# Kernel optimization log

Hardware: AMD Instinct MI355X
Metric: run time of the kernel (lower is better)

The kernel has to match this reference:

```python
import jax, jax.numpy as jnp
import numpy as np

N = 100000      # nodes (single ntype)
R = 4           # edge types (relations)
E = 160000      # edges per relation
D_IN = 128
D_OUT = 128


def setup_inputs() -> dict:
    key = jax.random.key(0)
    k1, k2, k3, k4, k5 = jax.random.split(key, 5)
    gain = np.sqrt(2.0)  # calculate_gain('relu')
    bound = gain * np.sqrt(6.0 / (D_IN + D_OUT))  # xavier_uniform
    return {
        "x": jax.random.normal(k1, (N, D_IN), dtype=jnp.float32),
        "weight": jax.random.uniform(k2, (R, D_IN, D_OUT), dtype=jnp.float32,
                                     minval=-bound, maxval=bound),
        "loop_weight": jax.random.uniform(k3, (D_IN, D_OUT), dtype=jnp.float32,
                                          minval=-bound, maxval=bound),
        "h_bias": jnp.zeros((D_OUT,), dtype=jnp.float32),
        "src_idx": jax.random.randint(k4, (R, E), 0, N),
        "dst_idx": jax.random.randint(k5, (R, E), 0, N),
    }


def reference(x, weight, loop_weight, h_bias, src_idx, dst_idx):
    # Per-relation GraphConv(norm='right', weight external):
    #   h_r = segment_sum((x @ W_r)[src], dst) / clamp(in_degree, 1)
    # HeteroGraphConv default aggregation sums relations per dst node.
    n = x.shape[0]
    xw = jnp.einsum('nd,rdo->rno', x, weight)  # [R, N, D_OUT]
    h = jnp.zeros((n, weight.shape[2]), dtype=x.dtype)
    ones = jnp.ones((src_idx.shape[1],), dtype=x.dtype)
    for r in range(weight.shape[0]):  # small fixed relation count
        msg = xw[r][src_idx[r]]                                   # [E, D_OUT]
        agg = jax.ops.segment_sum(msg, dst_idx[r], num_segments=n)
        deg = jax.ops.segment_sum(ones, dst_idx[r], num_segments=n)
        h = h + agg / jnp.clip(deg, 1.0)[:, None]                 # norm='right'
    # self-loop + bias + activation (dropout=0 -> identity)
    h = h + x @ loop_weight + h_bias
    return jax.nn.relu(h)
```

## Files before the change

### kernel.cpp

```cpp
#include <hip/hip_runtime.h>

#define DD 128
#define KY 512
#define KT 640
#define RR 4
#define BKT 16
#define CAPS 15
#define NKS (KT / 32)

typedef short short8 __attribute__((ext_vector_type(8)));
typedef float f32x4 __attribute__((ext_vector_type(4)));

union U4S8 { uint4 u; short8 s; };

__device__ __forceinline__ unsigned short f2bf(float f) {
  unsigned u = __float_as_uint(f);
  u += 0x7fffu + ((u >> 16) & 1u);
  return (unsigned short)(u >> 16);
}

__global__ __launch_bounds__(256) void prep(const float* __restrict__ x,
                                            const float* __restrict__ weight,
                                            const float* __restrict__ loopw,
                                            const int* __restrict__ src,
                                            const int* __restrict__ dst,
                                            unsigned short* __restrict__ xb,
                                            unsigned short* __restrict__ wt,
                                            int* __restrict__ slot,
                                            int N, int E, int FB, int XB) {
  int b = blockIdx.x;
  int t = threadIdx.x;
  if (b < FB) {
    int i = b * 256 + t;
    if (i >= RR * E) return;
    int r = i / E;
    size_t base = ((size_t)dst[i] * RR + r) * BKT;
    int pos = atomicAdd(slot + base, 1);
    if (pos < CAPS) slot[base + 1 + pos] = src[i];
  } else if (b < FB + XB) {
    int i = (b - FB) * 256 + t;
    if (i >= (N + 1) * 16) return;
    int n = i >> 4;
    uint4 o = make_uint4(0, 0, 0, 0);
    if (n < N) {
      const float4* xp = (const float4*)x + (size_t)i * 2;
      float4 v0 = xp[0], v1 = xp[1];
      o.x = (unsigned)f2bf(v0.x) | ((unsigned)f2bf(v0.y) << 16);
      o.y = (unsigned)f2bf(v0.z) | ((unsigned)f2bf(v0.w) << 16);
      o.z = (unsigned)f2bf(v1.x) | ((unsigned)f2bf(v1.y) << 16);
      o.w = (unsigned)f2bf(v1.z) | ((unsigned)f2bf(v1.w) << 16);
    }
    ((uint4*)xb)[i] = o;
  } else {
    int i = (b - FB - XB) * 256 + t;
    if (i >= DD * KT) return;
    int j = i & 7, l = (i >> 3) & 63, c = (i >> 9) & 7, ks = i >> 12;
    int k = ks * 32 + (l >> 4) * 8 + j;
    int col = c * 16 + (l & 15);
    float v = (k < KY) ? weight[(size_t)((k >> 7) * DD + (k & (DD - 1))) * DD + col]
                       : loopw[(size_t)(k - KY) * DD + col];
    wt[i] = f2bf(v);
  }
}

__global__ __launch_bounds__(256) void gather_agg(const unsigned* __restrict__ xbu,
                                                  const int* __restrict__ slot,
                                                  unsigned* __restrict__ yu,
                                                  int NN ) {
  int gid = blockIdx.x * 256 + threadIdx.x;
  int n = gid >> 6, lane = gid & 63;
  if (n >= NN) return;
  int N = NN - 1;

  int sv = slot[(size_t)n * 64 + lane];

  int cn[RR], ct[RR];
#pragma unroll
  for (int r = 0; r < RR; r++) {
    ct[r] = __builtin_amdgcn_readlane(sv, r << 4);
    cn[r] = ct[r] > CAPS ? CAPS : ct[r];
  }

  float ax[RR], ay[RR];
#pragma unroll
  for (int r = 0; r < RR; r++) { ax[r] = 0.f; ay[r] = 0.f; }

#pragma unroll
  for (int r = 0; r < RR; r++) {
    for (int u = 0; u < cn[r]; u += 2) {
      int s0 = __builtin_amdgcn_readlane(sv, (r << 4) + 1 + u);
      int s1 = __builtin_amdgcn_readlane(sv, (r << 4) + 2 + u);
      s1 = (u + 1 < cn[r]) ? s1 : N;
      unsigned v0 = xbu[(size_t)s0 * 64 + lane];
      unsigned v1 = xbu[(size_t)s1 * 64 + lane];
      ax[r] += __uint_as_float(v0 << 16);
      ay[r] += __uint_as_float(v0 & 0xffff0000u);
      ax[r] += __uint_as_float(v1 << 16);
      ay[r] += __uint_as_float(v1 & 0xffff0000u);
    }
  }

#pragma unroll
  for (int r = 0; r < RR; r++) {
    float inv = 1.0f / (float)max(ct[r], 1);
    yu[(size_t)n * (KY / 2) + r * 64 + lane] =
        (unsigned)f2bf(ax[r] * inv) | ((unsigned)f2bf(ay[r] * inv) << 16);
  }
}

__global__ __launch_bounds__(512) void gemm_mfma(const unsigned short* __restrict__ y,
                                                 const unsigned short* __restrict__ xb,
                                                 const uint4* __restrict__ wtv,
                                                 const float* __restrict__ bias,
                                                 float* __restrict__ out, int N) {
  __shared__ __align__(16) unsigned short Bs[2][4096];
  int t = threadIdx.x;
  int w = t >> 6, lane = t & 63;
  int m = lane & 15, q = lane >> 4;
  int rb = blockIdx.x * 256;

  int grow0 = rb + w * 32 + m, grow1 = grow0 + 16;
  int r0c = grow0 > N ? N : grow0;
  int r1c = grow1 > N ? N : grow1;
  const unsigned short* ay0 = y  + (size_t)r0c * KY + q * 8;
  const unsigned short* ay1 = y  + (size_t)r1c * KY + q * 8;
  const unsigned short* ax0 = xb + (size_t)r0c * DD + q * 8;
  const unsigned short* ax1 = xb + (size_t)r1c * DD + q * 8;

  *(uint4*)(&Bs[0][t * 8]) = wtv[t];
  __syncthreads();

  f32x4 acc[2][8];
#pragma unroll
  for (int i = 0; i < 2; i++)
#pragma unroll
    for (int c = 0; c < 8; c++) acc[i][c] = (f32x4){0.f, 0.f, 0.f, 0.f};

#pragma unroll
  for (int ks = 0; ks < NKS; ++ks) {
    const int buf = ks & 1;
    uint4 bs;
    if (ks + 1 < NKS) bs = wtv[(size_t)(ks + 1) * 512 + t];

    U4S8 a0, a1;
    if (ks < 16) {
      a0.u = *(const uint4*)(ay0 + ks * 32);
      a1.u = *(const uint4*)(ay1 + ks * 32);
    } else {
      a0.u = *(const uint4*)(ax0 + (ks - 16) * 32);
      a1.u = *(const uint4*)(ax1 + (ks - 16) * 32);
    }

    short8 bb[8];
#pragma unroll
    for (int c = 0; c < 8; ++c)
      bb[c] = *(const short8*)(&Bs[buf][(c * 64 + lane) * 8]);

#pragma unroll
    for (int c = 0; c < 8; ++c) {
      acc[0][c] = __builtin_amdgcn_mfma_f32_16x16x32_bf16(a0.s, bb[c], acc[0][c], 0, 0, 0);
      acc[1][c] = __builtin_amdgcn_mfma_f32_16x16x32_bf16(a1.s, bb[c], acc[1][c], 0, 0, 0);
    }

    if (ks + 1 < NKS) {
      *(uint4*)(&Bs[buf ^ 1][t * 8]) = bs;
      __syncthreads();
    }
  }

  float bv[8];
#pragma unroll
  for (int c = 0; c < 8; ++c) bv[c] = bias[c * 16 + m];
#pragma unroll
  for (int i = 0; i < 2; ++i) {
    int rbase = rb + w * 32 + i * 16 + q * 4;
#pragma unroll
    for (int v = 0; v < 4; ++v) {
      int gr = rbase + v;
      if (gr < N) {
#pragma unroll
        for (int c = 0; c < 8; ++c)
          out[(size_t)gr * DD + c * 16 + m] = fmaxf(acc[i][c][v] + bv[c], 0.f);
      }
    }
  }
}

extern "C" void kernel_launch(void* const* d_in, const int* in_sizes, int n_in,
                              void* d_out, int out_size, void* d_ws, size_t ws_size,
                              hipStream_t stream) {
  const float* x      = (const float*)d_in[0];
  const float* weight = (const float*)d_in[1];
  const float* loop_w = (const float*)d_in[2];
  const float* h_bias = (const float*)d_in[3];
  const int*   src    = (const int*)d_in[4];
  const int*   dst    = (const int*)d_in[5];
  float* out = (float*)d_out;

  const int N = in_sizes[0] / DD;
  const int R = in_sizes[1] / (DD * DD);
  const int E = in_sizes[4] / R;
  const int RE = R * E;

  char* p = (char*)d_ws;
  auto alloc = [&](size_t bytes) {
    char* q = p;
    p += (bytes + 63) & ~size_t(63);
    return q;
  };
  int* slot = (int*)alloc((size_t)(N + 1) * RR * BKT * 4);
  unsigned short* wt = (unsigned short*)alloc((size_t)DD * KT * 2);
  unsigned short* xb = (unsigned short*)alloc((size_t)(N + 1) * DD * 2);
  unsigned short* y  = (unsigned short*)alloc((size_t)(N + 1) * KY * 2);

  hipMemsetAsync(slot, 0, (size_t)(N + 1) * RR * BKT * 4, stream);

  int FB = (RE + 255) / 256;
  int XB = ((N + 1) * 16 + 255) / 256;
  int WB = (DD * KT + 255) / 256;
  prep<<<FB + XB + WB, 256, 0, stream>>>(x, weight, loop_w, src, dst,
                                         xb, wt, slot, N, E, FB, XB);
  gather_agg<<<((size_t)(N + 1) * 64 + 255) / 256, 256, 0, stream>>>(
      (const unsigned*)xb, slot, (unsigned*)y, N + 1);
  gemm_mfma<<<(N + 255) / 256, 512, 0, stream>>>(y, xb, (const uint4*)wt,
                                                 h_bias, out, N);
}
```

Measured before the change: 226.7 us.

## Fuse memset, prep, gather and GEMM into one cooperative persistent kernel

Replaces the memset and three separate kernel launches with a single cooperative kernel. Each stage becomes a grid-stride loop, and grid.sync() separates slot zeroing, bucketing/conversion, aggregation and the MFMA GEMM. The aim is to remove launch overhead and inter-kernel gaps. In exchange the grid is capped at 512 persistent blocks, adds three grid-wide barriers, and could lower parallelism in the gather stage compared with the earlier one-wave-per-node launch.

```diff
diff --git a/kernel.cpp b/kernel.cpp
--- a/kernel.cpp
+++ b/kernel.cpp
@@ -1,4 +1,7 @@
 #include <hip/hip_runtime.h>
+#include <hip/hip_cooperative_groups.h>
+
+namespace cg = cooperative_groups;
 
 #define DD 128
 #define KY 512
@@ -19,168 +22,171 @@
   return (unsigned short)(u >> 16);
 }
 
-__global__ __launch_bounds__(256) void prep(const float* __restrict__ x,
-                                            const float* __restrict__ weight,
-                                            const float* __restrict__ loopw,
-                                            const int* __restrict__ src,
-                                            const int* __restrict__ dst,
-                                            unsigned short* __restrict__ xb,
-                                            unsigned short* __restrict__ wt,
-                                            int* __restrict__ slot,
-                                            int N, int E, int FB, int XB) {
-  int b = blockIdx.x;
-  int t = threadIdx.x;
-  if (b < FB) {
-    int i = b * 256 + t;
-    if (i >= RR * E) return;
-    int r = i / E;
-    size_t base = ((size_t)dst[i] * RR + r) * BKT;
-    int pos = atomicAdd(slot + base, 1);
-    if (pos < CAPS) slot[base + 1 + pos] = src[i];
-  } else if (b < FB + XB) {
-    int i = (b - FB) * 256 + t;
-    if (i >= (N + 1) * 16) return;
-    int n = i >> 4;
-    uint4 o = make_uint4(0, 0, 0, 0);
-    if (n < N) {
-      const float4* xp = (const float4*)x + (size_t)i * 2;
-      float4 v0 = xp[0], v1 = xp[1];
-      o.x = (unsigned)f2bf(v0.x) | ((unsigned)f2bf(v0.y) << 16);
-      o.y = (unsigned)f2bf(v0.z) | ((unsigned)f2bf(v0.w) << 16);
-      o.z = (unsigned)f2bf(v1.x) | ((unsigned)f2bf(v1.y) << 16);
-      o.w = (unsigned)f2bf(v1.z) | ((unsigned)f2bf(v1.w) << 16);
-    }
-    ((uint4*)xb)[i] = o;
-  } else {
-    int i = (b - FB - XB) * 256 + t;
-    if (i >= DD * KT) return;
-    int j = i & 7, l = (i >> 3) & 63, c = (i >> 9) & 7, ks = i >> 12;
-    int k = ks * 32 + (l >> 4) * 8 + j;
-    int col = c * 16 + (l & 15);
-    float v = (k < KY) ? weight[(size_t)((k >> 7) * DD + (k & (DD - 1))) * DD + col]
-                       : loopw[(size_t)(k - KY) * DD + col];
-    wt[i] = f2bf(v);
-  }
-}
-
-__global__ __launch_bounds__(256) void gather_agg(const unsigned* __restrict__ xbu,
-                                                  const int* __restrict__ slot,
-                                                  unsigned* __restrict__ yu,
-                                                  int NN ) {
-  int gid = blockIdx.x * 256 + threadIdx.x;
-  int n = gid >> 6, lane = gid & 63;
-  if (n >= NN) return;
-  int N = NN - 1;
-
-  int sv = slot[(size_t)n * 64 + lane];
-
-  int cn[RR], ct[RR];
-#pragma unroll
-  for (int r = 0; r < RR; r++) {
-    ct[r] = __builtin_amdgcn_readlane(sv, r << 4);
-    cn[r] = ct[r] > CAPS ? CAPS : ct[r];
-  }
-
-  float ax[RR], ay[RR];
-#pragma unroll
-  for (int r = 0; r < RR; r++) { ax[r] = 0.f; ay[r] = 0.f; }
-
-#pragma unroll
-  for (int r = 0; r < RR; r++) {
-    for (int u = 0; u < cn[r]; u += 2) {
-      int s0 = __builtin_amdgcn_readlane(sv, (r << 4) + 1 + u);
-      int s1 = __builtin_amdgcn_readlane(sv, (r << 4) + 2 + u);
-      s1 = (u + 1 < cn[r]) ? s1 : N;
-      unsigned v0 = xbu[(size_t)s0 * 64 + lane];
-      unsigned v1 = xbu[(size_t)s1 * 64 + lane];
-      ax[r] += __uint_as_float(v0 << 16);
-      ay[r] += __uint_as_float(v0 & 0xffff0000u);
-      ax[r] += __uint_as_float(v1 << 16);
-      ay[r] += __uint_as_float(v1 & 0xffff0000u);
-    }
-  }
-
-#pragma unroll
-  for (int r = 0; r < RR; r++) {
-    float inv = 1.0f / (float)max(ct[r], 1);
-    yu[(size_t)n * (KY / 2) + r * 64 + lane] =
-        (unsigned)f2bf(ax[r] * inv) | ((unsigned)f2bf(ay[r] * inv) << 16);
-  }
-}
-
-__global__ __launch_bounds__(512) void gemm_mfma(const unsigned short* __restrict__ y,
-                                                 const unsigned short* __restrict__ xb,
-                                                 const uint4* __restrict__ wtv,
-                                                 const float* __restrict__ bias,
-                                                 float* __restrict__ out, int N) {
+__global__ __launch_bounds__(512, 4) void fused_all(
+    const float* __restrict__ x, const float* __restrict__ weight,
+    const float* __restrict__ loopw, const float* __restrict__ bias,
+    const int* __restrict__ src, const int* __restrict__ dst,
+    float* __restrict__ out, int* __restrict__ slot,
+    unsigned short* __restrict__ wt, unsigned short* __restrict__ xb,
+    unsigned short* __restrict__ y, int N, int E) {
   __shared__ __align__(16) unsigned short Bs[2][4096];
-  int t = threadIdx.x;
-  int w = t >> 6, lane = t & 63;
-  int m = lane & 15, q = lane >> 4;
-  int rb = blockIdx.x * 256;
-
-  int grow0 = rb + w * 32 + m, grow1 = grow0 + 16;
-  int r0c = grow0 > N ? N : grow0;
-  int r1c = grow1 > N ? N : grow1;
-  const unsigned short* ay0 = y  + (size_t)r0c * KY + q * 8;
-  const unsigned short* ay1 = y  + (size_t)r1c * KY + q * 8;
-  const unsigned short* ax0 = xb + (size_t)r0c * DD + q * 8;
-  const unsigned short* ax1 = xb + (size_t)r1c * DD + q * 8;
-
-  *(uint4*)(&Bs[0][t * 8]) = wtv[t];
-  __syncthreads();
-
-  f32x4 acc[2][8];
-#pragma unroll
-  for (int i = 0; i < 2; i++)
-#pragma unroll
-    for (int c = 0; c < 8; c++) acc[i][c] = (f32x4){0.f, 0.f, 0.f, 0.f};
-
-#pragma unroll
-  for (int ks = 0; ks < NKS; ++ks) {
-    const int buf = ks & 1;
-    uint4 bs;
-    if (ks + 1 < NKS) bs = wtv[(size_t)(ks + 1) * 512 + t];
-
-    U4S8 a0, a1;
-    if (ks < 16) {
-      a0.u = *(const uint4*)(ay0 + ks * 32);
-      a1.u = *(const uint4*)(ay1 + ks * 32);
-    } else {
-      a0.u = *(const uint4*)(ax0 + (ks - 16) * 32);
-      a1.u = *(const uint4*)(ax1 + (ks - 16) * 32);
-    }
-
-    short8 bb[8];
-#pragma unroll
-    for (int c = 0; c < 8; ++c)
-      bb[c] = *(const short8*)(&Bs[buf][(c * 64 + lane) * 8]);
-
-#pragma unroll
-    for (int c = 0; c < 8; ++c) {
-      acc[0][c] = __builtin_amdgcn_mfma_f32_16x16x32_bf16(a0.s, bb[c], acc[0][c], 0, 0, 0);
-      acc[1][c] = __builtin_amdgcn_mfma_f32_16x16x32_bf16(a1.s, bb[c], acc[1][c], 0, 0, 0);
-    }
-
-    if (ks + 1 < NKS) {
-      *(uint4*)(&Bs[buf ^ 1][t * 8]) = bs;
+  cg::grid_group grid = cg::this_grid();
+  const int t = threadIdx.x;
+  const int gtid = blockIdx.x * 512 + t;
+  const int GT = gridDim.x * 512;
+
+  {
+    const int tot = (N + 1) * 16;
+    const uint4 z = make_uint4(0, 0, 0, 0);
+    for (int i = gtid; i < tot; i += GT) ((uint4*)slot)[i] = z;
+  }
+  grid.sync();
+
+  {
+    const int RE = RR * E;
+    for (int i = gtid; i < RE; i += GT) {
+      int r = i / E;
+      size_t base = ((size_t)dst[i] * RR + r) * BKT;
+      int pos = atomicAdd(slot + base, 1);
+      if (pos < CAPS) slot[base + 1 + pos] = src[i];
+    }
+    const int XT = (N + 1) * 16;
+    for (int i = gtid; i < XT; i += GT) {
+      int n = i >> 4;
+      uint4 o = make_uint4(0, 0, 0, 0);
+      if (n < N) {
+        const float4* xp = (const float4*)x + (size_t)i * 2;
+        float4 v0 = xp[0], v1 = xp[1];
+        o.x = (unsigned)f2bf(v0.x) | ((unsigned)f2bf(v0.y) << 16);
+        o.y = (unsigned)f2bf(v0.z) | ((unsigned)f2bf(v0.w) << 16);
+        o.z = (unsigned)f2bf(v1.x) | ((unsigned)f2bf(v1.y) << 16);
+        o.w = (unsigned)f2bf(v1.z) | ((unsigned)f2bf(v1.w) << 16);
+      }
+      ((uint4*)xb)[i] = o;
+    }
+    for (int i = gtid; i < DD * KT; i += GT) {
+      int j = i & 7, l = (i >> 3) & 63, c = (i >> 9) & 7, ks = i >> 12;
+      int k = ks * 32 + (l >> 4) * 8 + j;
+      int col = c * 16 + (l & 15);
+      float v = (k < KY) ? weight[(size_t)((k >> 7) * DD + (k & (DD - 1))) * DD + col]
+                         : loopw[(size_t)(k - KY) * DD + col];
+      wt[i] = f2bf(v);
+    }
+  }
+  grid.sync();
+
+  {
+    const unsigned* xbu = (const unsigned*)xb;
+    unsigned* yu = (unsigned*)y;
+    const int wid = gtid >> 6, lane = gtid & 63;
+    const int NW = GT >> 6;
+    for (int n = wid; n <= N; n += NW) {
+      int sv = slot[(size_t)n * 64 + lane];
+      int cn[RR], ct[RR];
+#pragma unroll
+      for (int r = 0; r < RR; r++) {
+        ct[r] = __builtin_amdgcn_readlane(sv, r << 4);
+        cn[r] = ct[r] > CAPS ? CAPS : ct[r];
+      }
+      float ax[RR], ay[RR];
+#pragma unroll
+      for (int r = 0; r < RR; r++) { ax[r] = 0.f; ay[r] = 0.f; }
+#pragma unroll
+      for (int r = 0; r < RR; r++) {
+        for (int u = 0; u < cn[r]; u += 2) {
+          int s0 = __builtin_amdgcn_readlane(sv, (r << 4) + 1 + u);
+          int s1 = __builtin_amdgcn_readlane(sv, ((r << 4) + 2 + u) & 63);
+          s1 = (u + 1 < cn[r]) ? s1 : N;
+          unsigned v0 = xbu[(size_t)s0 * 64 + lane];
+          unsigned v1 = xbu[(size_t)s1 * 64 + lane];
+          ax[r] += __uint_as_float(v0 << 16);
+          ay[r] += __uint_as_float(v0 & 0xffff0000u);
+          ax[r] += __uint_as_float(v1 << 16);
+          ay[r] += __uint_as_float(v1 & 0xffff0000u);
+        }
+      }
+#pragma unroll
+      for (int r = 0; r < RR; r++) {
+        float inv = 1.0f / (float)max(ct[r], 1);
+        yu[(size_t)n * (KY / 2) + r * 64 + lane] =
+            (unsigned)f2bf(ax[r] * inv) | ((unsigned)f2bf(ay[r] * inv) << 16);
+      }
+    }
+  }
+  grid.sync();
+
+  {
+    const uint4* wtv = (const uint4*)wt;
+    const int w = t >> 6, lane = t & 63;
+    const int m = lane & 15, q = lane >> 4;
+    const int ntile = (N + 255) / 256;
+    for (int tile = blockIdx.x; tile < ntile; tile += gridDim.x) {
       __syncthreads();
-    }
-  }
-
-  float bv[8];
-#pragma unroll
-  for (int c = 0; c < 8; ++c) bv[c] = bias[c * 16 + m];
-#pragma unroll
-  for (int i = 0; i < 2; ++i) {
-    int rbase = rb + w * 32 + i * 16 + q * 4;
-#pragma unroll
-    for (int v = 0; v < 4; ++v) {
-      int gr = rbase + v;
-      if (gr < N) {
+      const int rb = tile * 256;
+      int grow0 = rb + w * 32 + m, grow1 = grow0 + 16;
+      int r0c = grow0 > N ? N : grow0;
+      int r1c = grow1 > N ? N : grow1;
+      const unsigned short* ay0 = y  + (size_t)r0c * KY + q * 8;
+      const unsigned short* ay1 = y  + (size_t)r1c * KY + q * 8;
+      const unsigned short* ax0 = xb + (size_t)r0c * DD + q * 8;
+      const unsigned short* ax1 = xb + (size_t)r1c * DD + q * 8;
+
+      *(uint4*)(&Bs[0][t * 8]) = wtv[t];
+      __syncthreads();
+
+      f32x4 acc[2][8];
+#pragma unroll
+      for (int i = 0; i < 2; i++)
+#pragma unroll
+        for (int c = 0; c < 8; c++) acc[i][c] = (f32x4){0.f, 0.f, 0.f, 0.f};
+
+#pragma unroll
+      for (int ks = 0; ks < NKS; ++ks) {
+        const int buf = ks & 1;
+        uint4 bs;
+        if (ks + 1 < NKS) bs = wtv[(size_t)(ks + 1) * 512 + t];
+
+        U4S8 a0, a1;
+        if (ks < 16) {
+          a0.u = *(const uint4*)(ay0 + ks * 32);
+          a1.u = *(const uint4*)(ay1 + ks * 32);
+        } else {
+          a0.u = *(const uint4*)(ax0 + (ks - 16) * 32);
+          a1.u = *(const uint4*)(ax1 + (ks - 16) * 32);
+        }
+
+        short8 bb[8];
 #pragma unroll
         for (int c = 0; c < 8; ++c)
-          out[(size_t)gr * DD + c * 16 + m] = fmaxf(acc[i][c][v] + bv[c], 0.f);
+          bb[c] = *(const short8*)(&Bs[buf][(c * 64 + lane) * 8]);
+
+#pragma unroll
+        for (int c = 0; c < 8; ++c) {
+          acc[0][c] = __builtin_amdgcn_mfma_f32_16x16x32_bf16(a0.s, bb[c], acc[0][c], 0, 0, 0);
+          acc[1][c] = __builtin_amdgcn_mfma_f32_16x16x32_bf16(a1.s, bb[c], acc[1][c], 0, 0, 0);
+        }
+
+        if (ks + 1 < NKS) {
+          *(uint4*)(&Bs[buf ^ 1][t * 8]) = bs;
+          __syncthreads();
+        }
+      }
+
+      float bv[8];
+#pragma unroll
+      for (int c = 0; c < 8; ++c) bv[c] = bias[c * 16 + m];
+#pragma unroll
+      for (int i = 0; i < 2; ++i) {
+        int rbase = rb + w * 32 + i * 16 + q * 4;
+#pragma unroll
+        for (int v = 0; v < 4; ++v) {
+          int gr = rbase + v;
+          if (gr < N) {
+#pragma unroll
+            for (int c = 0; c < 8; ++c)
+              out[(size_t)gr * DD + c * 16 + m] = fmaxf(acc[i][c][v] + bv[c], 0.f);
+          }
+        }
       }
     }
   }
@@ -197,10 +203,9 @@
   const int*   dst    = (const int*)d_in[5];
   float* out = (float*)d_out;
 
-  const int N = in_sizes[0] / DD;
+  int N = in_sizes[0] / DD;
   const int R = in_sizes[1] / (DD * DD);
-  const int E = in_sizes[4] / R;
-  const int RE = R * E;
+  int E = in_sizes[4] / R;
 
   char* p = (char*)d_ws;
   auto alloc = [&](size_t bytes) {
@@ -213,15 +218,19 @@
   unsigned short* xb = (unsigned short*)alloc((size_t)(N + 1) * DD * 2);
   unsigned short* y  = (unsigned short*)alloc((size_t)(N + 1) * KY * 2);
 
-  hipMemsetAsync(slot, 0, (size_t)(N + 1) * RR * BKT * 4, stream);
-
-  int FB = (RE + 255) / 256;
-  int XB = ((N + 1) * 16 + 255) / 256;
-  int WB = (DD * KT + 255) / 256;
-  prep<<<FB + XB + WB, 256, 0, stream>>>(x, weight, loop_w, src, dst,
-                                         xb, wt, slot, N, E, FB, XB);
-  gather_agg<<<((size_t)(N + 1) * 64 + 255) / 256, 256, 0, stream>>>(
-      (const unsigned*)xb, slot, (unsigned*)y, N + 1);
-  gemm_mfma<<<(N + 255) / 256, 512, 0, stream>>>(y, xb, (const uint4*)wt,
-                                                 h_bias, out, N);
+  static int gridn = 0;
+  if (gridn == 0) {
+    int per = 0;
+    if (hipOccupancyMaxActiveBlocksPerMultiprocessor(
+            &per, (const void*)fused_all, 512, 0) != hipSuccess || per < 1)
+      per = 1;
+    long g = (long)per * 256;
+    gridn = (int)(g > 512 ? 512 : g);
+  }
+
+  void* args[] = {(void*)&x, (void*)&weight, (void*)&loop_w, (void*)&h_bias,
+                  (void*)&src, (void*)&dst, (void*)&out, (void*)&slot,
+                  (void*)&wt, (void*)&xb, (void*)&y, (void*)&N, (void*)&E};
+  hipLaunchCooperativeKernel((const void*)fused_all, dim3(gridn), dim3(512),
+                             args, 0, stream);
 }
```

After: 417.3 us. +84.1%, slower.
